# Kernel tuning notes

Hardware: AMD Instinct MI355X
Metric: run time of the kernel (lower is better)

## Reference

```python
import jax, jax.numpy as jnp
import numpy as np

N = 50000      # nodes
E = 800000     # edges (avg degree 16)
IN = 512       # input features
OUT = 32       # per-head hidden features
H = 8          # heads (layer 1)
C = 16         # classes (layer 2, 1 head)
NEG_SLOPE = 0.2


def setup_inputs() -> dict:
    key = jax.random.key(0)
    ks = jax.random.split(key, 8)
    x = jax.random.normal(ks[0], (N, IN), jnp.float32)
    edge_index = jax.random.randint(ks[1], (2, E), 0, N, jnp.int32)
    # layer 1 params: W1 [IN, H*OUT], attention vectors a1_src/a1_dst [H, OUT]
    W1 = jax.random.normal(ks[2], (IN, H * OUT), jnp.float32) * (1.0 / np.sqrt(IN))
    a1_src = jax.random.normal(ks[3], (H, OUT), jnp.float32) * (1.0 / np.sqrt(OUT))
    a1_dst = jax.random.normal(ks[4], (H, OUT), jnp.float32) * (1.0 / np.sqrt(OUT))
    # layer 2 params: single head, W2 [H*OUT, C], a2_src/a2_dst [1, C]
    W2 = jax.random.normal(ks[5], (H * OUT, C), jnp.float32) * (1.0 / np.sqrt(H * OUT))
    a2_src = jax.random.normal(ks[6], (1, C), jnp.float32) * (1.0 / np.sqrt(C))
    a2_dst = jax.random.normal(ks[7], (1, C), jnp.float32) * (1.0 / np.sqrt(C))
    return {"x": x, "W1": W1, "a1_src": a1_src, "a1_dst": a1_dst,
            "W2": W2, "a2_src": a2_src, "a2_dst": a2_dst,
            "edge_index": edge_index}


def gat_layer(x, edge_index, W, a_src, a_dst, concat):
    """Standard GAT layer: e_ij = LeakyReLU(a_src.Wh_i + a_dst.Wh_j),
    softmax over incoming edges of each target node, scatter-aggregate."""
    n = x.shape[0]
    h_heads, f = a_src.shape
    h = (x @ W).reshape(n, h_heads, f)                      # [N, H, F]
    src, dst = edge_index[0], edge_index[1]
    es = jnp.einsum('nhf,hf->nh', h, a_src)                 # [N, H] per-node src scores
    ed = jnp.einsum('nhf,hf->nh', h, a_dst)                 # [N, H]
    e = jax.nn.leaky_relu(es[src] + ed[dst], NEG_SLOPE)     # [E, H] per-edge logits
    # segment softmax over edges grouped by dst node
    m = jax.ops.segment_max(e, dst, num_segments=n)         # [N, H]
    m = jnp.where(jnp.isfinite(m), m, 0.0)                  # empty segments -> -inf
    p = jnp.exp(e - m[dst])                                 # [E, H]
    s = jax.ops.segment_sum(p, dst, num_segments=n)         # [N, H]
    denom = s[dst]
    alpha = p / jnp.where(denom > 0, denom, 1.0)            # [E, H]
    msg = h[src] * alpha[:, :, None]                        # [E, H, F]
    out = jax.ops.segment_sum(msg, dst, num_segments=n)     # [N, H, F]
    if concat:
        return out.reshape(n, h_heads * f)
    return out.mean(axis=1)


def reference(x, W1, a1_src, a1_dst, W2, a2_src, a2_dst, edge_index):
    # dropout is identity in eval mode
    h = gat_layer(x, edge_index, W1, a1_src, a1_dst, concat=True)   # [N, H*OUT]
    h = jax.nn.elu(h)
    h = gat_layer(h, edge_index, W2, a2_src, a2_dst, concat=False)  # [N, C]
    return jax.nn.log_softmax(h, axis=1)
```

## Files before the change

### kernel.cpp

```cpp
#include <hip/hip_runtime.h>

#define NN 50000
#define EE 800000
#define KIN 512
#define HF 256
#define NH 8
#define FOUT 32
#define NC 16
#define NEG 0.2f
#define NB_SCAN 196

typedef unsigned short u16;
typedef __attribute__((ext_vector_type(8))) short shortx8;
typedef __attribute__((ext_vector_type(4))) float floatx4;
typedef __attribute__((ext_vector_type(8))) unsigned short ushortx8;
typedef __attribute__((ext_vector_type(4))) unsigned uintx4;

__device__ __forceinline__ float lrelu(float x) { return x > 0.f ? x : NEG * x; }

__device__ __forceinline__ u16 f2bf(float f) {
    unsigned u = __float_as_uint(f);
    return (u16)((u + 0x7FFFu + ((u >> 16) & 1u)) >> 16);
}
__device__ __forceinline__ float bf2f(u16 v) {
    return __uint_as_float((unsigned)v << 16);
}
__device__ __forceinline__ unsigned pk2bf(float a, float b) {
    unsigned ua = __float_as_uint(a), ub = __float_as_uint(b);
    return ((ua + 0x8000u) >> 16) | ((ub + 0x8000u) & 0xffff0000u);
}

__device__ __forceinline__ void gll16(const void* g, void* l) {
    __builtin_amdgcn_global_load_lds((const __attribute__((address_space(1))) void*)g,
                                     (__attribute__((address_space(3))) void*)l, 16, 0, 0);
}

__global__ void count_deg_convw(const int* __restrict__ dst, int* __restrict__ deg,
                                const float* __restrict__ W1, const float* __restrict__ W2,
                                u16* __restrict__ w1t, u16* __restrict__ w2t) {
    int e = blockIdx.x * 256 + threadIdx.x;
    if (e < EE) atomicAdd(&deg[dst[e]], 1);
    if (e < KIN * HF) {
        int k = e >> 8, n = e & 255;
        w1t[n * KIN + k] = f2bf(W1[e]);
    } else if (e < KIN * HF + HF * NC) {
        int e2 = e - KIN * HF;
        int k = e2 >> 4, c = e2 & 15;
        w2t[c * HF + k] = f2bf(W2[e2]);
    }
}

__global__ __launch_bounds__(256) void scan_a(const int* __restrict__ deg, int* __restrict__ bsum) {
    __shared__ int sm[256];
    int t = threadIdx.x;
    int i = blockIdx.x * 256 + t;
    sm[t] = (i < NN) ? deg[i] : 0;
    __syncthreads();
    for (int o = 128; o; o >>= 1) { if (t < o) sm[t] += sm[t + o]; __syncthreads(); }
    if (t == 0) bsum[blockIdx.x] = sm[0];
}

__global__ __launch_bounds__(256) void scan_c(const int* __restrict__ deg, const int* __restrict__ bsum,
                                              int* __restrict__ off) {
    __shared__ int sm[256];
    __shared__ int pre[256];
    int t = threadIdx.x;
    pre[t] = (t < blockIdx.x && t < NB_SCAN) ? bsum[t] : 0;
    __syncthreads();
    for (int o = 128; o; o >>= 1) { if (t < o) pre[t] += pre[t + o]; __syncthreads(); }
    int bofs = pre[0];
    __syncthreads();
    int i = blockIdx.x * 256 + t;
    int d = (i < NN) ? deg[i] : 0;
    sm[t] = d;
    __syncthreads();
    for (int dd = 1; dd < 256; dd <<= 1) {
        int v = (t >= dd) ? sm[t - dd] : 0;
        __syncthreads();
        sm[t] += v;
        __syncthreads();
    }
    if (i < NN) off[i] = bofs + sm[t] - d;
    if (i == 0) off[NN] = EE;
}

__global__ void fill_csr(const int* __restrict__ src, const int* __restrict__ dst,
                         const int* __restrict__ off, int* __restrict__ cursor,
                         int* __restrict__ csr_src) {
    int e = blockIdx.x * 256 + threadIdx.x;
    if (e < EE) {
        int d = dst[e];
        int pos = atomicAdd(&cursor[d], 1);
        csr_src[off[d] + pos] = src[e];
    }
}

__global__ __launch_bounds__(256, 3) void gemm1_mfma(const float* __restrict__ x,
                                                     const u16* __restrict__ w1t,
                                                     u16* __restrict__ h1b,
                                                     const float* __restrict__ a1s,
                                                     const float* __restrict__ a1d,
                                                     float* __restrict__ es1,
                                                     float* __restrict__ ed1) {
    __shared__ __align__(16) float As[8 * 64 * 4];
    __shared__ __align__(16) u16 Bs[4 * 256 * 8];
    int t = threadIdx.x;
    int lane = t & 63, wave = t >> 6;
    int wm = wave >> 1, wn = wave & 1;
    int lm = lane & 15, quad = lane >> 4;
    int bm = blockIdx.x * 64;

    floatx4 acc[2][8];
#pragma unroll
    for (int i = 0; i < 2; i++)
#pragma unroll
        for (int j = 0; j < 8; j++) acc[i][j] = (floatx4){0.f, 0.f, 0.f, 0.f};

    int arow = bm + lane;
    if (arow > NN - 1) arow = NN - 1;
    const float* axp = x + (size_t)arow * KIN;
    const u16* bxp[4];
#pragma unroll
    for (int b = 0; b < 4; b++) bxp[b] = w1t + (size_t)(b * 64 + lane) * KIN + wave * 8;

    for (int kk = 0; kk < KIN; kk += 32) {
#pragma unroll
        for (int a = 0; a < 2; a++) {
            int g = wave * 2 + a;
            gll16(axp + kk + g * 4, &As[g * 64 * 4]);
        }
#pragma unroll
        for (int b = 0; b < 4; b++)
            gll16(bxp[b] + kk, &Bs[(wave * 256 + b * 64) * 8]);
        __syncthreads();

        shortx8 af[2], bf[8];
#pragma unroll
        for (int i = 0; i < 2; i++) {
            int row = wm * 32 + i * 16 + lm;
            int g0 = quad * 2;
            float4 lo = *(const float4*)&As[(g0 * 64 + row) * 4];
            float4 hi = *(const float4*)&As[((g0 + 1) * 64 + row) * 4];
            union { uintx4 u; shortx8 s; } cv;
            cv.u[0] = pk2bf(lo.x, lo.y);
            cv.u[1] = pk2bf(lo.z, lo.w);
            cv.u[2] = pk2bf(hi.x, hi.y);
            cv.u[3] = pk2bf(hi.z, hi.w);
            af[i] = cv.s;
        }
#pragma unroll
        for (int j = 0; j < 8; j++) {
            int col = wn * 128 + j * 16 + lm;
            bf[j] = *(const shortx8*)&Bs[(quad * 256 + col) * 8];
        }
#pragma unroll
        for (int i = 0; i < 2; i++)
#pragma unroll
            for (int j = 0; j < 8; j++)
                acc[i][j] = __builtin_amdgcn_mfma_f32_16x16x32_bf16(af[i], bf[j], acc[i][j], 0, 0, 0);
        __syncthreads();
    }

#pragma unroll
    for (int i = 0; i < 2; i++) {
        int row = bm + wm * 32 + i * 16 + quad * 4;
#pragma unroll
        for (int j = 0; j < 8; j++) {
            int col = wn * 128 + j * 16 + lm;
#pragma unroll
            for (int r = 0; r < 4; r++) {
                if (row + r < NN) h1b[(size_t)(row + r) * HF + col] = f2bf(acc[i][j][r]);
            }
        }
    }

    float as_v[8], ad_v[8];
#pragma unroll
    for (int j = 0; j < 8; j++) {
        int col = wn * 128 + j * 16 + lm;
        as_v[j] = a1s[col];
        ad_v[j] = a1d[col];
    }
#pragma unroll
    for (int i = 0; i < 2; i++) {
#pragma unroll
        for (int r = 0; r < 4; r++) {
            int row = bm + wm * 32 + i * 16 + quad * 4 + r;
#pragma unroll
            for (int hp = 0; hp < 4; hp++) {
                float e_s = acc[i][2 * hp][r] * as_v[2 * hp] + acc[i][2 * hp + 1][r] * as_v[2 * hp + 1];
                float e_d = acc[i][2 * hp][r] * ad_v[2 * hp] + acc[i][2 * hp + 1][r] * ad_v[2 * hp + 1];
#pragma unroll
                for (int o = 8; o; o >>= 1) {
                    e_s += __shfl_down(e_s, o, 16);
                    e_d += __shfl_down(e_d, o, 16);
                }
                if (lm == 0 && row < NN) {
                    int h = wn * 4 + hp;
                    es1[row * NH + h] = e_s;
                    ed1[row * NH + h] = e_d;
                }
            }
        }
    }
}

__global__ __launch_bounds__(256) void agg1_mfma(const u16* __restrict__ h1b, const float* __restrict__ es,
                                                 const float* __restrict__ ed, const int* __restrict__ off,
                                                 const int* __restrict__ csr_src, u16* __restrict__ out1b) {
    __shared__ __align__(16) u16 Hs[32 * 256];
    __shared__ __align__(16) u16 pTs[8][32];
    __shared__ __align__(16) unsigned char dstloc[32];
    __shared__ int offs_s[17];
    __shared__ float ed_s[16][8];

    int t = threadIdx.x;
    int lane = t & 63, wave = t >> 6;
    int lm = lane & 15, quad = lane >> 4;
    int base = blockIdx.x * 16;

    if (t < 17) offs_s[t] = off[base + t];
    if (t < 128) ed_s[t >> 3][t & 7] = ed[(base + (t >> 3)) * NH + (t & 7)];
    int e0 = off[base];
    int e1 = off[base + 16];
    int nch = (e1 - e0 + 31) >> 5;
    __syncthreads();

    floatx4 acc[2][2];
    floatx4 accS[2];
#pragma unroll
    for (int a = 0; a < 2; a++) {
        accS[a] = (floatx4){0.f, 0.f, 0.f, 0.f};
#pragma unroll
        for (int b = 0; b < 2; b++) acc[a][b] = (floatx4){0.f, 0.f, 0.f, 0.f};
    }

    int h0 = 2 * wave;
    shortx8 ones;
#pragma unroll
    for (int i = 0; i < 8; i++) ones[i] = (short)0x3F80;

    int k_p = t >> 3, h_p = t & 7;
    int sv = 0;
    if (nch > 0) {
        int g = e0 + (lane & 31);
        sv = csr_src[g < e1 ? g : e1 - 1];
    }

    for (int c = 0; c < nch; c++) {
        int svn = 0;
        if (c + 1 < nch) {
            int g = e0 + ((c + 1) << 5) + (lane & 31);
            svn = csr_src[g < e1 ? g : e1 - 1];
        }
#pragma unroll
        for (int pass = 0; pass < 4; pass++) {
            int r = pass * 8 + 2 * wave + (lane >> 5);
            int s = __shfl(sv, r, 64);
            const u16* sp = h1b + (size_t)s * HF + (((lane & 31) ^ (pass << 1)) << 3);
            gll16(sp, Hs + pass * 2048 + wave * 512);
        }
        {
            int g = e0 + (c << 5) + k_p;
            int s = __shfl(sv, k_p, 64);
            float pv = 0.f;
            if (g < e1) {
                int m = 0;
                if (offs_s[m + 8] <= g) m += 8;
                if (offs_s[m + 4] <= g) m += 4;
                if (offs_s[m + 2] <= g) m += 2;
                if (offs_s[m + 1] <= g) m += 1;
                float lg = es[s * NH + h_p] + ed_s[m][h_p];
                lg = lg > 0.f ? lg : NEG * lg;
                pv = __expf(lg);
                if (h_p == 0) dstloc[k_p] = (unsigned char)m;
            }
            pTs[h_p][k_p] = f2bf(pv);
        }
        __syncthreads();

        union { uintx4 u; shortx8 s; } pa, pb, a0, a1;
        pa.s = *(const shortx8*)&pTs[h0][quad * 8];
        pb.s = *(const shortx8*)&pTs[h0 + 1][quad * 8];
        unsigned dw0 = *(const unsigned*)&dstloc[quad * 8];
        unsigned dw1 = *(const unsigned*)&dstloc[quad * 8 + 4];
        unsigned ulm = (unsigned)lm;
        unsigned mm0 = ((dw0 & 255u) == ulm ? 0xffffu : 0u) | (((dw0 >> 8) & 255u) == ulm ? 0xffff0000u : 0u);
        unsigned mm1 = (((dw0 >> 16) & 255u) == ulm ? 0xffffu : 0u) | ((dw0 >> 24) == ulm ? 0xffff0000u : 0u);
        unsigned mm2 = ((dw1 & 255u) == ulm ? 0xffffu : 0u) | (((dw1 >> 8) & 255u) == ulm ? 0xffff0000u : 0u);
        unsigned mm3 = (((dw1 >> 16) & 255u) == ulm ? 0xffffu : 0u) | ((dw1 >> 24) == ulm ? 0xffff0000u : 0u);
        a0.u[0] = pa.u[0] & mm0; a0.u[1] = pa.u[1] & mm1; a0.u[2] = pa.u[2] & mm2; a0.u[3] = pa.u[3] & mm3;
        a1.u[0] = pb.u[0] & mm0; a1.u[1] = pb.u[1] & mm1; a1.u[2] = pb.u[2] & mm2; a1.u[3] = pb.u[3] & mm3;

        accS[0] = __builtin_amdgcn_mfma_f32_16x16x32_bf16(a0.s, ones, accS[0], 0, 0, 0);
        accS[1] = __builtin_amdgcn_mfma_f32_16x16x32_bf16(a1.s, ones, accS[1], 0, 0, 0);

#pragma unroll
        for (int hh = 0; hh < 2; hh++) {
#pragma unroll
            for (int half = 0; half < 2; half++) {
                int f = (h0 + hh) * 32 + half * 16 + lm;
                int bidx = (quad * 8) * 256 + (((f >> 3) ^ (quad << 1)) << 3) + (f & 7);
                shortx8 bfv;
#pragma unroll
                for (int j = 0; j < 8; j++) bfv[j] = (short)Hs[bidx + j * 256];
                acc[hh][half] = __builtin_amdgcn_mfma_f32_16x16x32_bf16(
                    hh ? a1.s : a0.s, bfv, acc[hh][half], 0, 0, 0);
            }
        }
        __syncthreads();
        sv = svn;
    }

#pragma unroll
    for (int hh = 0; hh < 2; hh++) {
#pragma unroll
        for (int r = 0; r < 4; r++) {
            float sden = accS[hh][r];
            float inv = sden > 0.f ? 1.0f / sden : 0.f;
            int n = base + quad * 4 + r;
#pragma unroll
            for (int half = 0; half < 2; half++) {
                float v = acc[hh][half][r] * inv;
                v = v > 0.f ? v : (__expf(v) - 1.0f);
                out1b[(size_t)n * HF + (h0 + hh) * 32 + half * 16 + lm] = f2bf(v);
            }
        }
    }
}

__global__ __launch_bounds__(64) void gemm2_mfma(const u16* __restrict__ out1b, const u16* __restrict__ w2t,
                                                 const float* __restrict__ a2s, const float* __restrict__ a2d,
                                                 u16* __restrict__ h2b, float* __restrict__ es2,
                                                 float* __restrict__ ed2) {
    int lane = threadIdx.x;
    int lm = lane & 15, quad = lane >> 4;
    int nb = blockIdx.x * 16;
    floatx4 acc = (floatx4){0.f, 0.f, 0.f, 0.f};
    const u16* arow = out1b + (size_t)(nb + lm) * HF + quad * 8;
    const u16* brow = w2t + lm * HF + quad * 8;
#pragma unroll
    for (int kk = 0; kk < HF; kk += 32) {
        shortx8 af = *(const shortx8*)(arow + kk);
        shortx8 bf = *(const shortx8*)(brow + kk);
        acc = __builtin_amdgcn_mfma_f32_16x16x32_bf16(af, bf, acc, 0, 0, 0);
    }
    float a2sc = a2s[lm], a2dc = a2d[lm];
#pragma unroll
    for (int r = 0; r < 4; r++) {
        int n = nb + quad * 4 + r;
        float v = acc[r];
        h2b[n * NC + lm] = f2bf(v);
        float ps = v * a2sc, pd = v * a2dc;
#pragma unroll
        for (int o = 8; o; o >>= 1) {
            ps += __shfl_down(ps, o, 16);
            pd += __shfl_down(pd, o, 16);
        }
        if (lm == 0) { es2[n] = ps; ed2[n] = pd; }
    }
}

__global__ __launch_bounds__(256) void agg2(const u16* __restrict__ h2b, const float* __restrict__ es2,
                                            const float* __restrict__ ed2, const int* __restrict__ off,
                                            const int* __restrict__ csr_src, float* __restrict__ out) {
    int t = threadIdx.x;
    int nid = blockIdx.x * 16 + (t >> 4);
    int c = t & 15;
    int beg = off[nid];
    int deg = off[nid + 1] - beg;
    float edn = ed2[nid];
    float s = 0.f, acc = 0.f;
    for (int base = 0; base < deg; base += 16) {
        int nch = deg - base; if (nch > 16) nch = 16;
        int sv = 0;
        if (c < nch) sv = csr_src[beg + base + c];
        int sva[16];
#pragma unroll
        for (int e = 0; e < 16; e++) sva[e] = __shfl(sv, e, 16);
        float hva[16];
#pragma unroll
        for (int e = 0; e < 16; e++) hva[e] = bf2f(h2b[sva[e] * NC + c]);
        float p = 0.f;
        if (c < nch) p = __expf(lrelu(es2[sv] + edn));
        s += p;
        float pa[16];
#pragma unroll
        for (int e = 0; e < 16; e++) pa[e] = __shfl(p, e, 16);
#pragma unroll
        for (int e = 0; e < 16; e++) acc += pa[e] * hva[e];
    }
#pragma unroll
    for (int o = 8; o; o >>= 1) s += __shfl_down(s, o, 16);
    s = __shfl(s, 0, 16);
    float v = (s > 0.f) ? acc / s : 0.f;
    float m2 = v;
#pragma unroll
    for (int o = 8; o; o >>= 1) m2 = fmaxf(m2, __shfl_down(m2, o, 16));
    m2 = __shfl(m2, 0, 16);
    float se = __expf(v - m2);
#pragma unroll
    for (int o = 8; o; o >>= 1) se += __shfl_down(se, o, 16);
    se = __shfl(se, 0, 16);
    out[nid * NC + c] = v - m2 - __logf(se);
}

extern "C" void kernel_launch(void* const* d_in, const int* in_sizes, int n_in,
                              void* d_out, int out_size, void* d_ws, size_t ws_size,
                              hipStream_t stream) {
    const float* x   = (const float*)d_in[0];
    const float* W1  = (const float*)d_in[1];
    const float* a1s = (const float*)d_in[2];
    const float* a1d = (const float*)d_in[3];
    const float* W2  = (const float*)d_in[4];
    const float* a2s = (const float*)d_in[5];
    const float* a2d = (const float*)d_in[6];
    const int*   ei  = (const int*)d_in[7];
    const int* srcv = ei;
    const int* dstv = ei + EE;
    float* out = (float*)d_out;

    u16* h1b    = (u16*)d_ws;
    u16* out1b  = h1b + (size_t)NN * HF;
    float* es1  = (float*)(out1b + (size_t)NN * HF);
    float* ed1  = es1 + (size_t)NN * NH;
    u16* h2b    = (u16*)(ed1 + (size_t)NN * NH);
    float* es2v = (float*)(h2b + (size_t)NN * NC);
    float* ed2v = es2v + NN;
    int* deg    = (int*)(ed2v + NN);
    int* cursor = deg + NN;
    int* offs   = cursor + NN;
    int* csr    = offs + NN + 1;
    int* bsum   = csr + EE;
    u16* w1t    = (u16*)(bsum + 256);
    u16* w2t    = w1t + (size_t)HF * KIN;

    hipMemsetAsync(deg, 0, 2 * NN * sizeof(int), stream);
    count_deg_convw<<<(EE + 255) / 256, 256, 0, stream>>>(dstv, deg, W1, W2, w1t, w2t);
    scan_a<<<NB_SCAN, 256, 0, stream>>>(deg, bsum);
    scan_c<<<NB_SCAN, 256, 0, stream>>>(deg, bsum, offs);
    fill_csr<<<(EE + 255) / 256, 256, 0, stream>>>(srcv, dstv, offs, cursor, csr);
    gemm1_mfma<<<(NN + 63) / 64, 256, 0, stream>>>(x, w1t, h1b, a1s, a1d, es1, ed1);
    agg1_mfma<<<NN / 16, 256, 0, stream>>>(h1b, es1, ed1, offs, csr, out1b);
    gemm2_mfma<<<NN / 16, 64, 0, stream>>>(out1b, w2t, a2s, a2d, h2b, es2v, ed2v);
    agg2<<<NN / 16, 256, 0, stream>>>(h2b, es2v, ed2v, offs, csr, out);
}
```

Before: 394.1 us.

## Double-buffer LDS tiles in gemm1 to overlap global loads with MFMA

Splits the gemm1 shared-memory A and B tiles into two buffers and prefetches the next K-slice with direct global-to-LDS loads while the current slice is computed. It uses explicit vmcnt waits and scheduling barriers in place of __syncthreads. The goal is to hide global memory latency behind MFMA work. In exchange, LDS use per block doubles (about 32KB), which may limit occupancy at launch bounds of 3 blocks, and the manual waitcnt counting must match the number of loads issued per stage.

```diff
diff --git a/kernel.cpp b/kernel.cpp
--- a/kernel.cpp
+++ b/kernel.cpp
@@ -102,8 +102,10 @@
                                                      const float* __restrict__ a1d,
                                                      float* __restrict__ es1,
                                                      float* __restrict__ ed1) {
-    __shared__ __align__(16) float As[8 * 64 * 4];
-    __shared__ __align__(16) u16 Bs[4 * 256 * 8];
+    __shared__ __align__(16) float As0[8 * 64 * 4];
+    __shared__ __align__(16) float As1[8 * 64 * 4];
+    __shared__ __align__(16) u16 Bs0[4 * 256 * 8];
+    __shared__ __align__(16) u16 Bs1[4 * 256 * 8];
     int t = threadIdx.x;
     int lane = t & 63, wave = t >> 6;
     int wm = wave >> 1, wn = wave & 1;
@@ -123,43 +125,65 @@
 #pragma unroll
     for (int b = 0; b < 4; b++) bxp[b] = w1t + (size_t)(b * 64 + lane) * KIN + wave * 8;
 
-    for (int kk = 0; kk < KIN; kk += 32) {
-#pragma unroll
-        for (int a = 0; a < 2; a++) {
-            int g = wave * 2 + a;
-            gll16(axp + kk + g * 4, &As[g * 64 * 4]);
-        }
-#pragma unroll
-        for (int b = 0; b < 4; b++)
-            gll16(bxp[b] + kk, &Bs[(wave * 256 + b * 64) * 8]);
-        __syncthreads();
-
-        shortx8 af[2], bf[8];
-#pragma unroll
-        for (int i = 0; i < 2; i++) {
-            int row = wm * 32 + i * 16 + lm;
-            int g0 = quad * 2;
-            float4 lo = *(const float4*)&As[(g0 * 64 + row) * 4];
-            float4 hi = *(const float4*)&As[((g0 + 1) * 64 + row) * 4];
-            union { uintx4 u; shortx8 s; } cv;
-            cv.u[0] = pk2bf(lo.x, lo.y);
-            cv.u[1] = pk2bf(lo.z, lo.w);
-            cv.u[2] = pk2bf(hi.x, hi.y);
-            cv.u[3] = pk2bf(hi.z, hi.w);
-            af[i] = cv.s;
-        }
-#pragma unroll
-        for (int j = 0; j < 8; j++) {
-            int col = wn * 128 + j * 16 + lm;
-            bf[j] = *(const shortx8*)&Bs[(quad * 256 + col) * 8];
-        }
-#pragma unroll
-        for (int i = 0; i < 2; i++)
-#pragma unroll
-            for (int j = 0; j < 8; j++)
-                acc[i][j] = __builtin_amdgcn_mfma_f32_16x16x32_bf16(af[i], bf[j], acc[i][j], 0, 0, 0);
-        __syncthreads();
-    }
+#define G1_STAGE(AB, BB, KK)                                             \
+    {                                                                    \
+        _Pragma("unroll") for (int a = 0; a < 2; a++) {                  \
+            int g = wave * 2 + a;                                        \
+            gll16(axp + (KK) + g * 4, &AB[g * 64 * 4]);                  \
+        }                                                                \
+        _Pragma("unroll") for (int b = 0; b < 4; b++)                    \
+            gll16(bxp[b] + (KK), &BB[(wave * 256 + b * 64) * 8]);        \
+    }
+
+#define G1_WAITV(n) do { asm volatile("s_waitcnt vmcnt(" #n ")" ::: "memory"); \
+                         __builtin_amdgcn_sched_barrier(0); } while (0)
+#define G1_BAR() do { __builtin_amdgcn_sched_barrier(0);                 \
+                      __builtin_amdgcn_s_barrier();                      \
+                      __builtin_amdgcn_sched_barrier(0); } while (0)
+
+#define G1_COMPUTE(AB, BB)                                               \
+    {                                                                    \
+        shortx8 af[2], bfv[8];                                           \
+        _Pragma("unroll") for (int i = 0; i < 2; i++) {                  \
+            int row = wm * 32 + i * 16 + lm;                             \
+            int g0 = quad * 2;                                           \
+            float4 lo = *(const float4*)&AB[(g0 * 64 + row) * 4];        \
+            float4 hi = *(const float4*)&AB[((g0 + 1) * 64 + row) * 4];  \
+            union { uintx4 u; shortx8 s; } cv;                           \
+            cv.u[0] = pk2bf(lo.x, lo.y);                                 \
+            cv.u[1] = pk2bf(lo.z, lo.w);                                 \
+            cv.u[2] = pk2bf(hi.x, hi.y);                                 \
+            cv.u[3] = pk2bf(hi.z, hi.w);                                 \
+            af[i] = cv.s;                                                \
+        }                                                                \
+        _Pragma("unroll") for (int j = 0; j < 8; j++) {                  \
+            int col = wn * 128 + j * 16 + lm;                            \
+            bfv[j] = *(const shortx8*)&BB[(quad * 256 + col) * 8];       \
+        }                                                                \
+        _Pragma("unroll") for (int i = 0; i < 2; i++)                    \
+            _Pragma("unroll") for (int j = 0; j < 8; j++)                \
+                acc[i][j] = __builtin_amdgcn_mfma_f32_16x16x32_bf16(     \
+                    af[i], bfv[j], acc[i][j], 0, 0, 0);                  \
+    }
+
+    G1_STAGE(As0, Bs0, 0);
+#pragma unroll
+    for (int it = 0; it < 16; ++it) {
+        const int kk = it * 32;
+        if (it < 15) {
+            if (it & 1) { G1_STAGE(As0, Bs0, kk + 32); }
+            else        { G1_STAGE(As1, Bs1, kk + 32); }
+        }
+        if (it < 15) { G1_WAITV(6); } else { G1_WAITV(0); }
+        G1_BAR();
+        if (it & 1) { G1_COMPUTE(As1, Bs1); }
+        else        { G1_COMPUTE(As0, Bs0); }
+        G1_BAR();
+    }
+#undef G1_STAGE
+#undef G1_WAITV
+#undef G1_BAR
+#undef G1_COMPUTE
 
 #pragma unroll
     for (int i = 0; i < 2; i++) {
```

New measurement: 393.2 us. About the same (-0.2%).
